# Performance work log

Hardware: AMD Instinct MI355X
Metric: run time of the kernel (lower is better)

Reference implementation:

```python
import jax, jax.numpy as jnp
import numpy as np

UNITS = 512
GROUPS = 32
EPS = 1e-3  # keras GroupNormalization default epsilon


def group_norm(x, gamma, beta):
    # x: [B,H,W,C]; normalize over (H,W, channels-within-group)
    B, H, W, C = x.shape
    xg = x.reshape(B, H, W, GROUPS, C // GROUPS)
    mean = xg.mean(axis=(1, 2, 4), keepdims=True)
    var = xg.var(axis=(1, 2, 4), keepdims=True)
    xn = (xg - mean) * jax.lax.rsqrt(var + EPS)
    return xn.reshape(B, H, W, C) * gamma + beta


def setup_inputs() -> dict:
    key = jax.random.key(0)
    ks = jax.random.split(key, 6)
    B, H, W, C = 16, 32, 32, UNITS
    std = 0.02  # RandomNormal(stddev=0.02) kernel init
    return {
        "x": jax.random.normal(ks[0], (B, H, W, C), jnp.float32),
        "gamma": jnp.ones((C,), jnp.float32),
        "beta": jnp.zeros((C,), jnp.float32),
        "Wq": std * jax.random.normal(ks[1], (C, UNITS), jnp.float32),
        "bq": jnp.zeros((UNITS,), jnp.float32),
        "Wk": std * jax.random.normal(ks[2], (C, UNITS), jnp.float32),
        "bk": jnp.zeros((UNITS,), jnp.float32),
        "Wv": std * jax.random.normal(ks[3], (C, UNITS), jnp.float32),
        "bv": jnp.zeros((UNITS,), jnp.float32),
        "Wp": std * jax.random.normal(ks[4], (UNITS, UNITS), jnp.float32),
        "bp": jnp.zeros((UNITS,), jnp.float32),
    }


def reference(x, gamma, beta, Wq, bq, Wk, bk, Wv, bv, Wp, bp):
    B, H, W, C = x.shape
    scale = jnp.float32(UNITS) ** -0.5
    xn = group_norm(x, gamma, beta)  # note: original residual uses normalized input
    # flatten spatial dims to N = H*W tokens (same math as bhwc/bHWc einsums)
    xf = xn.reshape(B, H * W, C)
    q = xf @ Wq + bq
    k = xf @ Wk + bk
    v = xf @ Wv + bv
    scores = jnp.einsum('bnc,bmc->bnm', q, k) * scale  # [B, N, N]
    attn = jax.nn.softmax(scores, axis=-1)
    out = jnp.einsum('bnm,bmc->bnc', attn, v)
    proj = out @ Wp + bp
    return xn + proj.reshape(B, H, W, C)
```

## Files before the change

kernel.cpp:

```cpp
#include <hip/hip_runtime.h>
#include <math.h>

#define BATCH 16
#define NTOK  1024
#define CH    512
#define NGRP  32
#define GSZ   16
#define EPSV  1e-3f
#define MTOT  (BATCH*NTOK)
#define SCALE 0.04419417382415922f

typedef unsigned short u16;
typedef __attribute__((ext_vector_type(4))) float f32x4;
typedef __attribute__((ext_vector_type(8))) short s16x8;

__device__ __forceinline__ u16 f2bf(float f) {
    union { float f; unsigned u; } x{f};
    unsigned r = x.u + 0x7fff + ((x.u >> 16) & 1);
    return (u16)(r >> 16);
}
__device__ __forceinline__ u16 cvt_elem(float f)  { return f2bf(f); }
__device__ __forceinline__ u16 cvt_elem(u16 h)    { return h; }

__device__ __forceinline__ void gld16(const u16* g, u16* l) {
    __builtin_amdgcn_global_load_lds(
        (const __attribute__((address_space(1))) void*)g,
        (__attribute__((address_space(3))) void*)l, 16, 0, 0);
}

__global__ __launch_bounds__(256) void gn_stats(const float* __restrict__ x,
                                                float2* __restrict__ stats) {
    int bg = blockIdx.x;
    int b = bg >> 5, g = bg & 31;
    const float* base = x + (size_t)b * NTOK * CH + g * GSZ;
    float s = 0.f, ss = 0.f;
    for (int i = threadIdx.x; i < 4096; i += 256) {
        int p = i >> 2, c4 = i & 3;
        float4 v = *(const float4*)(base + (size_t)p * CH + c4 * 4);
        s  += v.x + v.y + v.z + v.w;
        ss += v.x * v.x + v.y * v.y + v.z * v.z + v.w * v.w;
    }
    for (int off = 32; off; off >>= 1) {
        s  += __shfl_down(s, off);
        ss += __shfl_down(ss, off);
    }
    __shared__ float2 part[4];
    if ((threadIdx.x & 63) == 0) part[threadIdx.x >> 6] = make_float2(s, ss);
    __syncthreads();
    if (threadIdx.x == 0) {
        float S = 0.f, SS = 0.f;
        for (int i = 0; i < 4; i++) { S += part[i].x; SS += part[i].y; }
        float mean = S * (1.f / 16384.f);
        float var  = SS * (1.f / 16384.f) - mean * mean;
        stats[bg] = make_float2(mean, rsqrtf(var + EPSV));
    }
}

__global__ __launch_bounds__(256) void gn_apply(const float* __restrict__ x,
                                                const float2* __restrict__ stats,
                                                const float* __restrict__ gamma,
                                                const float* __restrict__ beta,
                                                float* __restrict__ xn,
                                                u16* __restrict__ xnb) {
    size_t total = (size_t)MTOT * CH / 4;
    for (size_t i4 = (size_t)blockIdx.x * 256 + threadIdx.x; i4 < total;
         i4 += (size_t)gridDim.x * 256) {
        size_t flat = i4 * 4;
        int c = (int)(flat & (CH - 1));
        int b = (int)(flat >> 19);
        int g = c >> 4;
        float2 st = stats[(b << 5) + g];
        float4 xv = *(const float4*)(x + flat);
        float4 gv = *(const float4*)(gamma + c);
        float4 bv = *(const float4*)(beta + c);
        float4 o;
        o.x = (xv.x - st.x) * st.y * gv.x + bv.x;
        o.y = (xv.y - st.x) * st.y * gv.y + bv.y;
        o.z = (xv.z - st.x) * st.y * gv.z + bv.z;
        o.w = (xv.w - st.x) * st.y * gv.w + bv.w;
        *(float4*)(xn + flat) = o;
        uint2 h;
        h.x = (unsigned)f2bf(o.x) | ((unsigned)f2bf(o.y) << 16);
        h.y = (unsigned)f2bf(o.z) | ((unsigned)f2bf(o.w) << 16);
        *(uint2*)(xnb + flat) = h;
    }
}

template <typename TIN>
__global__ __launch_bounds__(256) void transpose_bf16(const TIN* __restrict__ in,
                                                      u16* __restrict__ out,
                                                      int R, int C, long sIn, long sOut) {
    __shared__ u16 tile[64][66];
    int z = blockIdx.z;
    in  += (size_t)z * sIn;
    out += (size_t)z * sOut;
    int r0 = blockIdx.y * 64, c0 = blockIdx.x * 64;
    int t = threadIdx.x;
    for (int i = 0; i < 16; i++) {
        int idx = i * 256 + t;
        int r = idx >> 6, c = idx & 63;
        tile[r][c] = cvt_elem(in[(size_t)(r0 + r) * C + c0 + c]);
    }
    __syncthreads();
    for (int i = 0; i < 16; i++) {
        int idx = i * 256 + t;
        int oc = idx >> 6, orr = idx & 63;
        out[(size_t)(c0 + oc) * R + r0 + orr] = tile[orr][oc];
    }
}

template <bool BIAS, bool RES, bool OUTF32>
__global__ __launch_bounds__(256) void gemm_bt(
    const u16* __restrict__ A, const u16* __restrict__ B, void* __restrict__ Cout,
    const float* __restrict__ bias, const float* __restrict__ res,
    int K, int lda, int ldb, int ldc,
    long sA, long sB, long sC, float alpha) {
    __shared__ __align__(16) u16 Asm[4096];
    __shared__ __align__(16) u16 Bsm[4096];
    int z = blockIdx.z;
    A += (size_t)z * sA;
    B += (size_t)z * sB;
    size_t zc = (size_t)z * sC;

    int t = threadIdx.x;
    int wave = t >> 6, lane = t & 63;
    int wm = wave >> 1, wn = wave & 1;
    int rowA0 = blockIdx.y * 128;
    int colB0 = blockIdx.x * 128;

    int c16log = (lane & 3) ^ ((lane >> 3) & 3);
    const u16* aG[2]; const u16* bG[2]; u16* aL[2]; u16* bL[2];
#pragma unroll
    for (int j = 0; j < 2; j++) {
        int s = wave * 2 + j;
        int row = s * 16 + (lane >> 2);
        aL[j] = Asm + s * 512;
        bL[j] = Bsm + s * 512;
        aG[j] = A + (size_t)(rowA0 + row) * lda + c16log * 8;
        bG[j] = B + (size_t)(colB0 + row) * ldb + c16log * 8;
    }

    int kg = lane >> 4;
    int aoff[4], boff[4];
#pragma unroll
    for (int i = 0; i < 4; i++) {
        int ra = wm * 64 + i * 16 + (lane & 15);
        aoff[i] = ra * 32 + (kg ^ ((ra >> 1) & 3)) * 8;
        int rb = wn * 64 + i * 16 + (lane & 15);
        boff[i] = rb * 32 + (kg ^ ((rb >> 1) & 3)) * 8;
    }

    f32x4 acc[4][4] = {};
    for (int kt = 0; kt < K; kt += 32) {
        gld16(aG[0] + kt, aL[0]);
        gld16(aG[1] + kt, aL[1]);
        gld16(bG[0] + kt, bL[0]);
        gld16(bG[1] + kt, bL[1]);
        __syncthreads();
        s16x8 af[4], bfr[4];
#pragma unroll
        for (int i = 0; i < 4; i++) {
            af[i]  = *(const s16x8*)(Asm + aoff[i]);
            bfr[i] = *(const s16x8*)(Bsm + boff[i]);
        }
#pragma unroll
        for (int mi = 0; mi < 4; mi++)
#pragma unroll
            for (int nj = 0; nj < 4; nj++)
                acc[mi][nj] = __builtin_amdgcn_mfma_f32_16x16x32_bf16(
                    af[mi], bfr[nj], acc[mi][nj], 0, 0, 0);
        __syncthreads();
    }

    int r0 = rowA0 + wm * 64 + (lane >> 4) * 4;
    int c0c = colB0 + wn * 64 + (lane & 15);
#pragma unroll
    for (int mi = 0; mi < 4; mi++) {
#pragma unroll
        for (int nj = 0; nj < 4; nj++) {
            int c = c0c + nj * 16;
            float bv = BIAS ? bias[c] : 0.f;
            f32x4 v = acc[mi][nj];
#pragma unroll
            for (int j = 0; j < 4; j++) {
                int rr = r0 + mi * 16 + j;
                float val = v[j] * alpha + bv;
                if (RES) val += res[(size_t)rr * ldc + c];
                if (OUTF32) ((float*)Cout)[zc + (size_t)rr * ldc + c] = val;
                else        ((u16*)Cout)[zc + (size_t)rr * ldc + c] = f2bf(val);
            }
        }
    }
}

__global__ __launch_bounds__(256) void softmax_rows(const float* __restrict__ s,
                                                    u16* __restrict__ P) {
    size_t row = blockIdx.x;
    const float* p = s + row * 1024;
    int t = threadIdx.x;
    float4 v = *(const float4*)(p + t * 4);
    float m = fmaxf(fmaxf(v.x, v.y), fmaxf(v.z, v.w));
    for (int off = 32; off; off >>= 1) m = fmaxf(m, __shfl_xor(m, off));
    __shared__ float redm[4], reds[4];
    if ((t & 63) == 0) redm[t >> 6] = m;
    __syncthreads();
    m = fmaxf(fmaxf(redm[0], redm[1]), fmaxf(redm[2], redm[3]));
    v.x = __expf(v.x - m); v.y = __expf(v.y - m);
    v.z = __expf(v.z - m); v.w = __expf(v.w - m);
    float sum = v.x + v.y + v.z + v.w;
    for (int off = 32; off; off >>= 1) sum += __shfl_xor(sum, off);
    if ((t & 63) == 0) reds[t >> 6] = sum;
    __syncthreads();
    float inv = 1.f / (reds[0] + reds[1] + reds[2] + reds[3]);
    uint2 h;
    h.x = (unsigned)f2bf(v.x * inv) | ((unsigned)f2bf(v.y * inv) << 16);
    h.y = (unsigned)f2bf(v.z * inv) | ((unsigned)f2bf(v.w * inv) << 16);
    *(uint2*)(P + row * 1024 + t * 4) = h;
}

extern "C" void kernel_launch(void* const* d_in, const int* in_sizes, int n_in,
                              void* d_out, int out_size, void* d_ws, size_t ws_size,
                              hipStream_t stream) {
    const float* x     = (const float*)d_in[0];
    const float* gamma = (const float*)d_in[1];
    const float* beta  = (const float*)d_in[2];
    const float* Wq    = (const float*)d_in[3];
    const float* bq    = (const float*)d_in[4];
    const float* Wk    = (const float*)d_in[5];
    const float* bk    = (const float*)d_in[6];
    const float* Wv    = (const float*)d_in[7];
    const float* bv    = (const float*)d_in[8];
    const float* Wp    = (const float*)d_in[9];
    const float* bp    = (const float*)d_in[10];
    float* out = (float*)d_out;

    const size_t SZ  = (size_t)MTOT * CH;
    const size_t NSZ = (size_t)NTOK * CH;
    const size_t SCB = (size_t)NTOK * NTOK;

    char* p = (char*)d_ws;
    float*  xn    = (float*)p;           p += SZ * 4;
    float2* stats = (float2*)p;          p += 512 * sizeof(float2);
    p = (char*)(((size_t)p + 255) & ~(size_t)255);
    u16* WTq = (u16*)p;                  p += CH * CH * 2;
    u16* WTk = (u16*)p;                  p += CH * CH * 2;
    u16* WTv = (u16*)p;                  p += CH * CH * 2;
    u16* WTp = (u16*)p;                  p += CH * CH * 2;
    u16* xnb = (u16*)p;                  p += SZ * 2;
    u16* qb  = (u16*)p;                  p += SZ * 2;
    u16* kb  = (u16*)p;                  p += SZ * 2;
    u16* vb  = (u16*)p;                  p += SZ * 2;
    u16* vt  = (u16*)p;                  p += SZ * 2;
    u16* ao  = (u16*)p;                  p += SZ * 2;
    u16* P   = (u16*)p;                  p += (size_t)BATCH * SCB * 2;
    float* sc = (float*)p;
    size_t used = (size_t)(p - (char*)d_ws);
    bool full = ws_size >= used + (size_t)BATCH * SCB * 4;

    dim3 blk(256);

    gn_stats<<<BATCH * NGRP, blk, 0, stream>>>(x, stats);
    gn_apply<<<2048, blk, 0, stream>>>(x, stats, gamma, beta, xn, xnb);

    transpose_bf16<float><<<dim3(8, 8, 1), blk, 0, stream>>>(Wq, WTq, CH, CH, 0, 0);
    transpose_bf16<float><<<dim3(8, 8, 1), blk, 0, stream>>>(Wk, WTk, CH, CH, 0, 0);
    transpose_bf16<float><<<dim3(8, 8, 1), blk, 0, stream>>>(Wv, WTv, CH, CH, 0, 0);
    transpose_bf16<float><<<dim3(8, 8, 1), blk, 0, stream>>>(Wp, WTp, CH, CH, 0, 0);

    gemm_bt<true, false, false><<<dim3(4, 128, 1), blk, 0, stream>>>(
        xnb, WTq, qb, bq, nullptr, CH, CH, CH, CH, 0, 0, 0, 1.f);
    gemm_bt<true, false, false><<<dim3(4, 128, 1), blk, 0, stream>>>(
        xnb, WTk, kb, bk, nullptr, CH, CH, CH, CH, 0, 0, 0, 1.f);
    gemm_bt<true, false, false><<<dim3(4, 128, 1), blk, 0, stream>>>(
        xnb, WTv, vb, bv, nullptr, CH, CH, CH, CH, 0, 0, 0, 1.f);

    transpose_bf16<u16><<<dim3(8, 16, BATCH), blk, 0, stream>>>(
        vb, vt, NTOK, CH, (long)NSZ, (long)NSZ);

    if (full) {
        gemm_bt<false, false, true><<<dim3(8, 8, BATCH), blk, 0, stream>>>(
            qb, kb, sc, nullptr, nullptr, CH, CH, CH, NTOK,
            (long)NSZ, (long)NSZ, (long)SCB, SCALE);
        softmax_rows<<<BATCH * NTOK, blk, 0, stream>>>(sc, P);
    } else {
        for (int b = 0; b < BATCH; b++) {
            gemm_bt<false, false, true><<<dim3(8, 8, 1), blk, 0, stream>>>(
                qb + b * NSZ, kb + b * NSZ, sc, nullptr, nullptr,
                CH, CH, CH, NTOK, 0, 0, 0, SCALE);
            softmax_rows<<<NTOK, blk, 0, stream>>>(sc, P + b * SCB);
        }
    }

    gemm_bt<false, false, false><<<dim3(4, 8, BATCH), blk, 0, stream>>>(
        P, vt, ao, nullptr, nullptr, NTOK, NTOK, NTOK, CH,
        (long)SCB, (long)NSZ, (long)NSZ, 1.f);

    gemm_bt<true, true, true><<<dim3(4, 128, 1), blk, 0, stream>>>(
        ao, WTp, out, bp, xn, CH, CH, CH, CH, 0, 0, 0, 1.f);
}
```

Measured before the change: 311.7 us.

## Fuse QKV projections and QK^T with softmax into a single attention-score kernel

Merges the three Q/K/V projection GEMMs into one GEMM writing an interleaved QKV buffer, and collapses the four weight transposes into one launch. Computes QK^T and the row softmax in one kernel that keeps each 64x1024 score tile in registers and writes only the bf16 probabilities. This removes the fp32 score matrix round trip through global memory. It also remaps GEMM block indices in an XCD-interleaved order to improve L2 locality. The cost is a heavy-register kernel with only 256 blocks of 512 threads, which risks low occupancy and a serialized K-load loop.

```diff
diff --git a/kernel.cpp b/kernel.cpp
--- a/kernel.cpp
+++ b/kernel.cpp
@@ -9,6 +9,7 @@
 #define EPSV  1e-3f
 #define MTOT  (BATCH*NTOK)
 #define SCALE 0.04419417382415922f
+#define SEXP  (SCALE*1.4426950408889634f)
 
 typedef unsigned short u16;
 typedef __attribute__((ext_vector_type(4))) float f32x4;
@@ -19,8 +20,6 @@
     unsigned r = x.u + 0x7fff + ((x.u >> 16) & 1);
     return (u16)(r >> 16);
 }
-__device__ __forceinline__ u16 cvt_elem(float f)  { return f2bf(f); }
-__device__ __forceinline__ u16 cvt_elem(u16 h)    { return h; }
 
 __device__ __forceinline__ void gld16(const u16* g, u16* l) {
     __builtin_amdgcn_global_load_lds(
@@ -86,10 +85,39 @@
     }
 }
 
-template <typename TIN>
-__global__ __launch_bounds__(256) void transpose_bf16(const TIN* __restrict__ in,
-                                                      u16* __restrict__ out,
-                                                      int R, int C, long sIn, long sOut) {
+__global__ __launch_bounds__(256) void weights_prep(
+    const float* __restrict__ Wq, const float* __restrict__ Wk,
+    const float* __restrict__ Wv, const float* __restrict__ Wp,
+    u16* __restrict__ WTqkv, u16* __restrict__ WTp) {
+    int z = blockIdx.z;
+    const float* src = z == 0 ? Wq : z == 1 ? Wk : z == 2 ? Wv : Wp;
+    u16* dst = z < 3 ? WTqkv + (size_t)z * CH * CH : WTp;
+    __shared__ u16 tile[64][66];
+    int r0 = blockIdx.y * 64, c0 = blockIdx.x * 64;
+    int t = threadIdx.x;
+    for (int i = 0; i < 16; i++) {
+        int idx = i * 256 + t;
+        int r = idx >> 6, c = idx & 63;
+        tile[r][c] = f2bf(src[(size_t)(r0 + r) * CH + c0 + c]);
+    }
+    __syncthreads();
+    for (int i = 0; i < 16; i++) {
+        int idx = i * 256 + t;
+        int oc = idx >> 6, orr = idx & 63;
+        dst[(size_t)(c0 + oc) * CH + r0 + orr] = tile[orr][oc];
+    }
+}
+
+__global__ void prep_bias(const float* __restrict__ bq, const float* __restrict__ bk,
+                          const float* __restrict__ bv, float* __restrict__ bqkv) {
+    int t = blockIdx.x * 256 + threadIdx.x;
+    bqkv[t] = t < 512 ? bq[t] : (t < 1024 ? bk[t - 512] : bv[t - 1024]);
+}
+
+__global__ __launch_bounds__(256) void vt_transpose(const u16* __restrict__ in,
+                                                    u16* __restrict__ out,
+                                                    int R, int C, int ldIn,
+                                                    long sIn, long sOut) {
     __shared__ u16 tile[64][66];
     int z = blockIdx.z;
     in  += (size_t)z * sIn;
@@ -99,7 +127,7 @@
     for (int i = 0; i < 16; i++) {
         int idx = i * 256 + t;
         int r = idx >> 6, c = idx & 63;
-        tile[r][c] = cvt_elem(in[(size_t)(r0 + r) * C + c0 + c]);
+        tile[r][c] = in[(size_t)(r0 + r) * ldIn + c0 + c];
     }
     __syncthreads();
     for (int i = 0; i < 16; i++) {
@@ -117,16 +145,23 @@
     long sA, long sB, long sC, float alpha) {
     __shared__ __align__(16) u16 Asm[4096];
     __shared__ __align__(16) u16 Bsm[4096];
-    int z = blockIdx.z;
-    A += (size_t)z * sA;
-    B += (size_t)z * sB;
-    size_t zc = (size_t)z * sC;
+
+    unsigned flat = blockIdx.x + gridDim.x * (blockIdx.y + gridDim.y * blockIdx.z);
+    unsigned nb = gridDim.x * gridDim.y * gridDim.z;
+    unsigned lf = (flat & 7) * (nb >> 3) + (flat >> 3);
+    unsigned pb = gridDim.x * gridDim.y;
+    unsigned bz = lf / pb, rem = lf - bz * pb;
+    unsigned by = rem / gridDim.x, bx = rem - by * gridDim.x;
+
+    A += (size_t)bz * sA;
+    B += (size_t)bz * sB;
+    size_t zc = (size_t)bz * sC;
 
     int t = threadIdx.x;
     int wave = t >> 6, lane = t & 63;
     int wm = wave >> 1, wn = wave & 1;
-    int rowA0 = blockIdx.y * 128;
-    int colB0 = blockIdx.x * 128;
+    int rowA0 = by * 128;
+    int colB0 = bx * 128;
 
     int c16log = (lane & 3) ^ ((lane >> 3) & 3);
     const u16* aG[2]; const u16* bG[2]; u16* aL[2]; u16* bL[2];
@@ -193,29 +228,126 @@
     }
 }
 
-__global__ __launch_bounds__(256) void softmax_rows(const float* __restrict__ s,
-                                                    u16* __restrict__ P) {
-    size_t row = blockIdx.x;
-    const float* p = s + row * 1024;
-    int t = threadIdx.x;
-    float4 v = *(const float4*)(p + t * 4);
-    float m = fmaxf(fmaxf(v.x, v.y), fmaxf(v.z, v.w));
-    for (int off = 32; off; off >>= 1) m = fmaxf(m, __shfl_xor(m, off));
-    __shared__ float redm[4], reds[4];
-    if ((t & 63) == 0) redm[t >> 6] = m;
+__global__ __launch_bounds__(512, 2) void attn_fused(const u16* __restrict__ qkv,
+                                                     u16* __restrict__ P) {
+    __shared__ __align__(16) u16 Bsm[32768];
+
+    unsigned flat = blockIdx.x;
+    unsigned lf = (flat & 7) * 32 + (flat >> 3);
+    int b = lf >> 4, mt = lf & 15;
+
+    int t = threadIdx.x, w = t >> 6, lane = t & 63;
+    int wr = w >> 1, wn = w & 1;
+    int l15 = lane & 15, kg = lane >> 4;
+
+    const u16* qbase = qkv + ((size_t)b * NTOK + mt * 64) * (3 * CH);
+    const u16* kbase = qkv + (size_t)b * NTOK * (3 * CH) + CH;
+
+    const u16* qrow = qbase + (size_t)(wr * 16 + l15) * (3 * CH) + kg * 8;
+    s16x8 aq[16];
+#pragma unroll
+    for (int kt = 0; kt < 16; kt++) aq[kt] = *(const s16x8*)(qrow + kt * 32);
+
+    int c16log = (lane & 3) ^ ((lane >> 3) & 3);
+    const u16* bG[8];
+#pragma unroll
+    for (int j = 0; j < 8; j++) {
+        int row = (w * 8 + j) * 16 + (lane >> 2);
+        bG[j] = kbase + (size_t)row * (3 * CH) + c16log * 8;
+    }
+    int rb0 = wn * 512 + l15;
+    int boff = rb0 * 32 + (kg ^ ((rb0 >> 1) & 3)) * 8;
+
+    f32x4 acc[32];
+#pragma unroll
+    for (int i = 0; i < 32; i++) acc[i] = f32x4{0.f, 0.f, 0.f, 0.f};
+
+#pragma unroll
+    for (int kt = 0; kt < 16; kt++) {
+#pragma unroll
+        for (int j = 0; j < 8; j++)
+            gld16(bG[j] + kt * 32, Bsm + (w * 8 + j) * 512);
+        __syncthreads();
+#pragma unroll
+        for (int nj = 0; nj < 32; nj++) {
+            s16x8 bf = *(const s16x8*)(Bsm + boff + nj * 512);
+            acc[nj] = __builtin_amdgcn_mfma_f32_16x16x32_bf16(aq[kt], bf, acc[nj], 0, 0, 0);
+        }
+        __syncthreads();
+    }
+
+    float* redm = (float*)Bsm;
+    float* reds = (float*)(Bsm + 256);
+
+    float mrow[4], inv[4], srow[4];
+#pragma unroll
+    for (int j = 0; j < 4; j++) {
+        float m = acc[0][j];
+#pragma unroll
+        for (int nj = 1; nj < 32; nj++) m = fmaxf(m, acc[nj][j]);
+        for (int off = 1; off < 16; off <<= 1) m = fmaxf(m, __shfl_xor(m, off));
+        mrow[j] = m;
+    }
+    if (l15 == 0) {
+#pragma unroll
+        for (int j = 0; j < 4; j++) redm[(wr * 16 + kg * 4 + j) * 2 + wn] = mrow[j];
+    }
     __syncthreads();
-    m = fmaxf(fmaxf(redm[0], redm[1]), fmaxf(redm[2], redm[3]));
-    v.x = __expf(v.x - m); v.y = __expf(v.y - m);
-    v.z = __expf(v.z - m); v.w = __expf(v.w - m);
-    float sum = v.x + v.y + v.z + v.w;
-    for (int off = 32; off; off >>= 1) sum += __shfl_xor(sum, off);
-    if ((t & 63) == 0) reds[t >> 6] = sum;
+#pragma unroll
+    for (int j = 0; j < 4; j++) {
+        int row = wr * 16 + kg * 4 + j;
+        mrow[j] = fmaxf(redm[row * 2], redm[row * 2 + 1]);
+    }
+#pragma unroll
+    for (int j = 0; j < 4; j++) {
+        float s = 0.f;
+#pragma unroll
+        for (int nj = 0; nj < 32; nj++) {
+            float e = exp2f((acc[nj][j] - mrow[j]) * SEXP);
+            acc[nj][j] = e;
+            s += e;
+        }
+        for (int off = 1; off < 16; off <<= 1) s += __shfl_xor(s, off);
+        srow[j] = s;
+    }
+    if (l15 == 0) {
+#pragma unroll
+        for (int j = 0; j < 4; j++) reds[(wr * 16 + kg * 4 + j) * 2 + wn] = srow[j];
+    }
     __syncthreads();
-    float inv = 1.f / (reds[0] + reds[1] + reds[2] + reds[3]);
-    uint2 h;
-    h.x = (unsigned)f2bf(v.x * inv) | ((unsigned)f2bf(v.y * inv) << 16);
-    h.y = (unsigned)f2bf(v.z * inv) | ((unsigned)f2bf(v.w * inv) << 16);
-    *(uint2*)(P + row * 1024 + t * 4) = h;
+#pragma unroll
+    for (int j = 0; j < 4; j++) {
+        int row = wr * 16 + kg * 4 + j;
+        inv[j] = 1.f / (reds[row * 2] + reds[row * 2 + 1]);
+    }
+
+    size_t pbase = (size_t)b * NTOK * NTOK + (size_t)mt * 64 * NTOK;
+#pragma unroll
+    for (int h = 0; h < 2; h++) {
+        __syncthreads();
+        if (wn == h) {
+#pragma unroll
+            for (int nj = 0; nj < 32; nj++) {
+                int c = nj * 16 + l15;
+                int c16 = c >> 3, cw = c & 7;
+#pragma unroll
+                for (int j = 0; j < 4; j++) {
+                    int row = wr * 16 + kg * 4 + j;
+                    int pc16 = c16 ^ ((row >> 2) & 7);
+                    Bsm[row * 512 + pc16 * 8 + cw] = f2bf(acc[nj][j] * inv[j]);
+                }
+            }
+        }
+        __syncthreads();
+#pragma unroll
+        for (int i = 0; i < 8; i++) {
+            int flat16 = (i * 512 + t) * 8;
+            int row = flat16 >> 9, c = flat16 & 511;
+            int pc16 = (c >> 3) ^ ((row >> 2) & 7);
+            uint4 vv = *(const uint4*)(Bsm + row * 512 + pc16 * 8);
+            *(uint4*)(P + pbase + (size_t)row * NTOK + h * 512 + c) = vv;
+        }
+    }
 }
 
 extern "C" void kernel_launch(void* const* d_in, const int* in_sizes, int n_in,
@@ -239,57 +371,31 @@
     const size_t SCB = (size_t)NTOK * NTOK;
 
     char* p = (char*)d_ws;
-    float*  xn    = (float*)p;           p += SZ * 4;
-    float2* stats = (float2*)p;          p += 512 * sizeof(float2);
-    p = (char*)(((size_t)p + 255) & ~(size_t)255);
-    u16* WTq = (u16*)p;                  p += CH * CH * 2;
-    u16* WTk = (u16*)p;                  p += CH * CH * 2;
-    u16* WTv = (u16*)p;                  p += CH * CH * 2;
-    u16* WTp = (u16*)p;                  p += CH * CH * 2;
-    u16* xnb = (u16*)p;                  p += SZ * 2;
-    u16* qb  = (u16*)p;                  p += SZ * 2;
-    u16* kb  = (u16*)p;                  p += SZ * 2;
-    u16* vb  = (u16*)p;                  p += SZ * 2;
-    u16* vt  = (u16*)p;                  p += SZ * 2;
-    u16* ao  = (u16*)p;                  p += SZ * 2;
-    u16* P   = (u16*)p;                  p += (size_t)BATCH * SCB * 2;
-    float* sc = (float*)p;
-    size_t used = (size_t)(p - (char*)d_ws);
-    bool full = ws_size >= used + (size_t)BATCH * SCB * 4;
+    float*  xn    = (float*)p;   p += SZ * 4;
+    u16*    xnb   = (u16*)p;     p += SZ * 2;
+    u16*    qkvb  = (u16*)p;     p += (size_t)MTOT * 3 * CH * 2;
+    u16*    vt    = (u16*)p;     p += SZ * 2;
+    u16*    ao    = (u16*)p;     p += SZ * 2;
+    u16*    P     = (u16*)p;     p += (size_t)BATCH * SCB * 2;
+    u16*    WTqkv = (u16*)p;     p += (size_t)3 * CH * CH * 2;
+    u16*    WTp   = (u16*)p;     p += (size_t)CH * CH * 2;
+    float*  bqkv  = (float*)p;   p += 3 * CH * 4;
+    float2* stats = (float2*)p;
 
     dim3 blk(256);
 
     gn_stats<<<BATCH * NGRP, blk, 0, stream>>>(x, stats);
     gn_apply<<<2048, blk, 0, stream>>>(x, stats, gamma, beta, xn, xnb);
-
-    transpose_bf16<float><<<dim3(8, 8, 1), blk, 0, stream>>>(Wq, WTq, CH, CH, 0, 0);
-    transpose_bf16<float><<<dim3(8, 8, 1), blk, 0, stream>>>(Wk, WTk, CH, CH, 0, 0);
-    transpose_bf16<float><<<dim3(8, 8, 1), blk, 0, stream>>>(Wv, WTv, CH, CH, 0, 0);
-    transpose_bf16<float><<<dim3(8, 8, 1), blk, 0, stream>>>(Wp, WTp, CH, CH, 0, 0);
-
-    gemm_bt<true, false, false><<<dim3(4, 128, 1), blk, 0, stream>>>(
-        xnb, WTq, qb, bq, nullptr, CH, CH, CH, CH, 0, 0, 0, 1.f);
-    gemm_bt<true, false, false><<<dim3(4, 128, 1), blk, 0, stream>>>(
-        xnb, WTk, kb, bk, nullptr, CH, CH, CH, CH, 0, 0, 0, 1.f);
-    gemm_bt<true, false, false><<<dim3(4, 128, 1), blk, 0, stream>>>(
-        xnb, WTv, vb, bv, nullptr, CH, CH, CH, CH, 0, 0, 0, 1.f);
-
-    transpose_bf16<u16><<<dim3(8, 16, BATCH), blk, 0, stream>>>(
-        vb, vt, NTOK, CH, (long)NSZ, (long)NSZ);
-
-    if (full) {
-        gemm_bt<false, false, true><<<dim3(8, 8, BATCH), blk, 0, stream>>>(
-            qb, kb, sc, nullptr, nullptr, CH, CH, CH, NTOK,
-            (long)NSZ, (long)NSZ, (long)SCB, SCALE);
-        softmax_rows<<<BATCH * NTOK, blk, 0, stream>>>(sc, P);
-    } else {
-        for (int b = 0; b < BATCH; b++) {
-            gemm_bt<false, false, true><<<dim3(8, 8, 1), blk, 0, stream>>>(
-                qb + b * NSZ, kb + b * NSZ, sc, nullptr, nullptr,
-                CH, CH, CH, NTOK, 0, 0, 0, SCALE);
-            softmax_rows<<<NTOK, blk, 0, stream>>>(sc, P + b * SCB);
-        }
-    }
+    weights_prep<<<dim3(8, 8, 4), blk, 0, stream>>>(Wq, Wk, Wv, Wp, WTqkv, WTp);
+    prep_bias<<<6, blk, 0, stream>>>(bq, bk, bv, bqkv);
+
+    gemm_bt<true, false, false><<<dim3(12, 128, 1), blk, 0, stream>>>(
+        xnb, WTqkv, qkvb, bqkv, nullptr, CH, CH, CH, 3 * CH, 0, 0, 0, 1.f);
+
+    vt_transpose<<<dim3(8, 16, BATCH), blk, 0, stream>>>(
+        qkvb + 2 * CH, vt, NTOK, CH, 3 * CH, (long)NTOK * 3 * CH, (long)NSZ);
+
+    attn_fused<<<256, 512, 0, stream>>>(qkvb, P);
 
     gemm_bt<false, false, false><<<dim3(4, 8, BATCH), blk, 0, stream>>>(
         P, vt, ao, nullptr, nullptr, NTOK, NTOK, NTOK, CH,
```

Result: faster. 270.0 us (-13.4%).
